# Optimization experiments

Measured on AMD Instinct MI355X. Metric: run time of the kernel, lower is better.

## Reference

```python
import jax, jax.numpy as jnp
import numpy as np

N, E, IN, C, H = 50000, 1600000, 128, 64, 2
HC = H * C  # 128; num_out = 128, conv_out channels per head = 64
NEG_SLOPE = 0.2


def setup_inputs() -> dict:
    key = jax.random.key(0)
    ks = jax.random.split(key, 16)
    x = jax.random.normal(ks[0], (N, IN), dtype=jnp.float32)
    edge_index = jax.random.randint(ks[1], (2, E), 0, N, dtype=jnp.int64)

    def gat_params(k, fan_in, heads, out_ch):
        k1, k2, k3 = jax.random.split(k, 3)
        sc = 1.0 / np.sqrt(fan_in)
        W = jax.random.normal(k1, (fan_in, heads * out_ch), dtype=jnp.float32) * sc
        a_src = jax.random.normal(k2, (heads, out_ch), dtype=jnp.float32) * 0.1
        a_dst = jax.random.normal(k3, (heads, out_ch), dtype=jnp.float32) * 0.1
        b = jnp.zeros((heads * out_ch,), dtype=jnp.float32)
        return W, a_src, a_dst, b

    W_in, a_src_in, a_dst_in, b_in = gat_params(ks[2], IN, H, C)
    # 2 hidden layers, stacked on leading axis
    Wh, ash, adh, bh = [], [], [], []
    for i in range(2):
        W, a_s, a_d, b = gat_params(ks[3 + i], HC, H, C)
        Wh.append(W); ash.append(a_s); adh.append(a_d); bh.append(b)
    W_h = jnp.stack(Wh); a_src_h = jnp.stack(ash)
    a_dst_h = jnp.stack(adh); b_h = jnp.stack(bh)
    W_out, a_src_out, a_dst_out, b_out = gat_params(ks[6], HC, H, C)
    return dict(x=x, edge_index=edge_index,
                W_in=W_in, a_src_in=a_src_in, a_dst_in=a_dst_in, b_in=b_in,
                W_h=W_h, a_src_h=a_src_h, a_dst_h=a_dst_h, b_h=b_h,
                W_out=W_out, a_src_out=a_src_out, a_dst_out=a_dst_out, b_out=b_out)


def gat_layer(xf, src, dst, W, a_src, a_dst, b, heads, out_ch):
    n = xf.shape[0]
    h = (xf @ W).reshape(n, heads, out_ch)              # [N,H,C]
    e_src = jnp.einsum('nhc,hc->nh', h, a_src)          # [N,H]
    e_dst = jnp.einsum('nhc,hc->nh', h, a_dst)
    e = jax.nn.leaky_relu(e_src[src] + e_dst[dst], NEG_SLOPE)  # [E',H]
    m = jax.ops.segment_max(e, dst, num_segments=n)     # softmax over edges per dst
    p = jnp.exp(e - m[dst])
    s = jax.ops.segment_sum(p, dst, num_segments=n)
    alpha = p / (s[dst] + 1e-16)
    out = jax.ops.segment_sum(alpha[:, :, None] * h[src], dst, num_segments=n)
    return out.reshape(n, heads * out_ch) + b


def reference(x, edge_index, W_in, a_src_in, a_dst_in, b_in,
              W_h, a_src_h, a_dst_h, b_h,
              W_out, a_src_out, a_dst_out, b_out):
    # add self loops (PyG GATConv default add_self_loops=True)
    loops = jnp.arange(N, dtype=edge_index.dtype)
    src = jnp.concatenate([edge_index[0], loops])
    dst = jnp.concatenate([edge_index[1], loops])

    h = jax.nn.relu(gat_layer(x, src, dst, W_in, a_src_in, a_dst_in, b_in, H, C))
    for i in range(2):
        h = jax.nn.relu(gat_layer(h, src, dst, W_h[i], a_src_h[i], a_dst_h[i], b_h[i], H, C))
    out = gat_layer(h, src, dst, W_out, a_src_out, a_dst_out, b_out, H, C)
    return out
```

## Files before the change

### kernel.cpp

```cpp
#include <hip/hip_runtime.h>

#define NNODES 50000
#define NEDGES 1600000
#define NEG_SLOPE 0.2f

#define SCAN_NB 256
#define SCAN_CH 196

#define MT_ROWS 64
#define NMT 782
#define GEMM_BLOCKS 768
#define COUNT_BLOCKS 256

typedef __attribute__((ext_vector_type(8))) short short8;
typedef __attribute__((ext_vector_type(4))) float f32x4;
typedef __attribute__((ext_vector_type(8))) _Float16 h16x8;
typedef __attribute__((ext_vector_type(8))) unsigned short us8;

static __device__ __forceinline__ unsigned short f2bf(float f) {
    unsigned u = __float_as_uint(f);
    unsigned r = u + 0x7FFFu + ((u >> 16) & 1u);
    return (unsigned short)(r >> 16);
}
static __device__ __forceinline__ float bf2f(unsigned short h) {
    return __uint_as_float(((unsigned)h) << 16);
}
static __device__ __forceinline__ unsigned short f2h(float f) {
    union { _Float16 x; unsigned short u; } c;
    c.x = (_Float16)f;
    return c.u;
}


__global__ __launch_bounds__(256) void k_bsum(const int* __restrict__ count,
                                              int* __restrict__ bsum) {
    __shared__ int red[4];
    int t = threadIdx.x, b = blockIdx.x;
    int idx = b * SCAN_CH + t;
    int v = (t < SCAN_CH && idx < NNODES) ? count[idx] + 1 : 0;
    #pragma unroll
    for (int m = 1; m <= 32; m <<= 1) v += __shfl_xor(v, m);
    if ((t & 63) == 0) red[t >> 6] = v;
    __syncthreads();
    if (t == 0) bsum[b] = red[0] + red[1] + red[2] + red[3];
}

__global__ __launch_bounds__(256) void k_bscan(const int* __restrict__ bsum,
                                               int* __restrict__ boff,
                                               int* __restrict__ row_ptr) {
    __shared__ int s[256];
    int t = threadIdx.x;
    int v = bsum[t];
    s[t] = v;
    __syncthreads();
    for (int off = 1; off < 256; off <<= 1) {
        int u = (t >= off) ? s[t - off] : 0;
        __syncthreads();
        s[t] += u;
        __syncthreads();
    }
    boff[t] = s[t] - v;
    if (t == 255) row_ptr[NNODES] = s[255];
}

__global__ __launch_bounds__(256) void k_rowptr(const int* __restrict__ count,
                                                const int* __restrict__ boff,
                                                int* __restrict__ row_ptr,
                                                int* __restrict__ csr_src) {
    __shared__ int s[256];
    int t = threadIdx.x, b = blockIdx.x;
    int idx = b * SCAN_CH + t;
    bool valid = (t < SCAN_CH && idx < NNODES);
    int v = valid ? count[idx] + 1 : 0;
    s[t] = v;
    __syncthreads();
    for (int off = 1; off < 256; off <<= 1) {
        int u = (t >= off) ? s[t - off] : 0;
        __syncthreads();
        s[t] += u;
        __syncthreads();
    }
    if (valid) {
        int run = boff[b] + s[t] - v;
        row_ptr[idx] = run;
        csr_src[run] = idx;
    }
}

__global__ void k_scatter(const int* __restrict__ ei, const int* __restrict__ row_ptr,
                          const int* __restrict__ pos, int* __restrict__ csr_src) {
    int t = blockIdx.x * blockDim.x + threadIdx.x;
    int stride = gridDim.x * blockDim.x;
    #pragma unroll
    for (int i = 0; i < 4; i++) {
        int e = t + i * stride;
        if (e < NEDGES) {
            int s = ei[e];
            int d = ei[NEDGES + e];
            __builtin_nontemporal_store(s, &csr_src[row_ptr[d] + 1 + pos[e]]);
        }
    }
}

__global__ __launch_bounds__(256) void k_wprep(const float* __restrict__ W0,
                                               const float* __restrict__ Wh,
                                               const float* __restrict__ Wout,
                                               unsigned short* __restrict__ wthi,
                                               unsigned short* __restrict__ wtlo) {
    int t = blockIdx.x * blockDim.x + threadIdx.x;
    int l = t >> 14;
    int i = t & 16383;
    int k = i >> 7, n = i & 127;
    const float* src = (l == 0) ? W0 : (l == 3) ? Wout : (Wh + (size_t)(l - 1) * 16384);
    float v = src[i];
    unsigned short h = f2bf(v);
    wthi[(size_t)l * 16384 + n * 128 + k] = h;
    wtlo[(size_t)l * 16384 + n * 128 + k] = f2bf(v - bf2f(h));
}

__global__ __launch_bounds__(256, 3) void k_gemm_mfma(
        const float* __restrict__ X,
        const unsigned short* __restrict__ Ahi, const unsigned short* __restrict__ Alo,
        const unsigned short* __restrict__ Wthi, const unsigned short* __restrict__ Wtlo,
        const float* __restrict__ a_src, const float* __restrict__ a_dst,
        unsigned short* __restrict__ Hh,
        float* __restrict__ e_src, float* __restrict__ e_dst, int use_x,
        const int* __restrict__ ei, int* __restrict__ count, int* __restrict__ pos)
{
    __shared__ __align__(16) short sAhi[MT_ROWS * 128];
    __shared__ __align__(16) short sAlo[MT_ROWS * 128];
    __shared__ float eS[4][MT_ROWS];
    __shared__ float eD[4][MT_ROWS];

    if (blockIdx.x >= GEMM_BLOCKS) {
        int t = (blockIdx.x - GEMM_BLOCKS) * 256 + threadIdx.x;
        for (int base = t; base < NEDGES; base += 8 * 65536) {
            #pragma unroll
            for (int i = 0; i < 8; i++) {
                int e = base + i * 65536;
                if (e < NEDGES) pos[e] = atomicAdd(&count[ei[NEDGES + e]], 1);
            }
        }
        return;
    }

    const int tid  = threadIdx.x;
    const int lane = tid & 63;
    const int w    = tid >> 6;
    const int l15  = lane & 15;
    const int quad = lane >> 4;

    short8 Bh[2][4], Bl[2][4];
    #pragma unroll
    for (int nt = 0; nt < 2; nt++) {
        int n = w * 32 + nt * 16 + l15;
        #pragma unroll
        for (int ks = 0; ks < 4; ks++) {
            Bh[nt][ks] = *(const short8*)(Wthi + (size_t)n * 128 + ks * 32 + quad * 8);
            Bl[nt][ks] = *(const short8*)(Wtlo + (size_t)n * 128 + ks * 32 + quad * 8);
        }
    }
    float as0 = a_src[w * 32 + l15],      ad0 = a_dst[w * 32 + l15];
    float as1 = a_src[w * 32 + 16 + l15], ad1 = a_dst[w * 32 + 16 + l15];

    for (int mt0 = blockIdx.x; mt0 < NMT; mt0 += GEMM_BLOCKS) {
        const int row0 = mt0 * MT_ROWS;

        for (int i = tid; i < MT_ROWS * 16; i += 256) {
            int m  = i >> 4;
            int kc = i & 15;
            int g  = row0 + m; if (g > NNODES - 1) g = NNODES - 1;
            int cp = kc ^ (m & 15);
            short8 vh, vl;
            if (use_x) {
                float4 xa = *(const float4*)(X + (size_t)g * 128 + kc * 8);
                float4 xb = *(const float4*)(X + (size_t)g * 128 + kc * 8 + 4);
                float xs[8] = {xa.x, xa.y, xa.z, xa.w, xb.x, xb.y, xb.z, xb.w};
                #pragma unroll
                for (int q = 0; q < 8; q++) {
                    unsigned short h = f2bf(xs[q]);
                    vh[q] = (short)h;
                    vl[q] = (short)f2bf(xs[q] - bf2f(h));
                }
            } else {
                vh = *(const short8*)(Ahi + (size_t)g * 128 + kc * 8);
                vl = *(const short8*)(Alo + (size_t)g * 128 + kc * 8);
            }
            *(short8*)&sAhi[m * 128 + cp * 8] = vh;
            *(short8*)&sAlo[m * 128 + cp * 8] = vl;
        }
        __syncthreads();

        f32x4 zero = {0.f, 0.f, 0.f, 0.f};
        f32x4 acc[4][2];
        #pragma unroll
        for (int mt = 0; mt < 4; mt++) { acc[mt][0] = zero; acc[mt][1] = zero; }
        #pragma unroll
        for (int mt = 0; mt < 4; mt++) {
            int m = mt * 16 + l15;
            #pragma unroll
            for (int ks = 0; ks < 4; ks++) {
                int kc = ks * 4 + quad;
                int cp = kc ^ l15;
                short8 ah = *(const short8*)&sAhi[m * 128 + cp * 8];
                short8 al = *(const short8*)&sAlo[m * 128 + cp * 8];
                #pragma unroll
                for (int nt = 0; nt < 2; nt++) {
                    acc[mt][nt] = __builtin_amdgcn_mfma_f32_16x16x32_bf16(ah, Bh[nt][ks], acc[mt][nt], 0, 0, 0);
                    acc[mt][nt] = __builtin_amdgcn_mfma_f32_16x16x32_bf16(al, Bh[nt][ks], acc[mt][nt], 0, 0, 0);
                    acc[mt][nt] = __builtin_amdgcn_mfma_f32_16x16x32_bf16(ah, Bl[nt][ks], acc[mt][nt], 0, 0, 0);
                }
            }
        }

        #pragma unroll
        for (int mt = 0; mt < 4; mt++) {
            #pragma unroll
            for (int r = 0; r < 4; r++) {
                int m = mt * 16 + quad * 4 + r;
                int g = row0 + m;
                float v0 = acc[mt][0][r], v1 = acc[mt][1][r];
                if (g < NNODES) {
                    int n0 = w * 32 + l15;
                    Hh[(size_t)g * 128 + n0]      = f2h(v0);
                    Hh[(size_t)g * 128 + n0 + 16] = f2h(v1);
                }
                float ps = v0 * as0 + v1 * as1;
                float pd = v0 * ad0 + v1 * ad1;
                ps += __shfl_xor(ps, 1); ps += __shfl_xor(ps, 2);
                ps += __shfl_xor(ps, 4); ps += __shfl_xor(ps, 8);
                pd += __shfl_xor(pd, 1); pd += __shfl_xor(pd, 2);
                pd += __shfl_xor(pd, 4); pd += __shfl_xor(pd, 8);
                if (l15 == 0) { eS[w][m] = ps; eD[w][m] = pd; }
            }
        }
        __syncthreads();
        if (tid < MT_ROWS * 2) {
            int m = tid >> 1, head = tid & 1;
            int g = row0 + m;
            if (g < NNODES) {
                e_src[g * 2 + head] = eS[head * 2][m] + eS[head * 2 + 1][m];
                e_dst[g * 2 + head] = eD[head * 2][m] + eD[head * 2 + 1][m];
            }
        }
        __syncthreads();
    }
}

template <int FINAL>
__device__ __forceinline__ void agg_body(const _Float16* __restrict__ Hh,
                                         const float* __restrict__ e_src,
                                         const float* __restrict__ e_dst,
                                         const int* __restrict__ row_ptr,
                                         const int* __restrict__ csr_src,
                                         const float* __restrict__ bias,
                                         float* __restrict__ outf,
                                         unsigned short* __restrict__ ohi,
                                         unsigned short* __restrict__ olo) {
    int lane = threadIdx.x & 63;
    int wv   = threadIdx.x >> 6;
    int d    = blockIdx.x * 4 + wv;
    if (d >= NNODES) return;
    int qt   = lane >> 4;
    int cl   = lane & 15;
    int head = cl >> 3;
    int c0   = cl * 8;
    float ed = e_dst[d * 2 + head];
    int beg = row_ptr[d], end = row_ptr[d + 1];
    float acc[8] = {0.f, 0.f, 0.f, 0.f, 0.f, 0.f, 0.f, 0.f};
    float ssum = 0.f;
    int j = beg;
    for (; j + 16 <= end; j += 16) {
        int s0 = csr_src[j + qt],      s1 = csr_src[j + 4 + qt];
        int s2 = csr_src[j + 8 + qt],  s3 = csr_src[j + 12 + qt];
        h16x8 h0 = *(const h16x8*)(Hh + (size_t)s0 * 128 + c0);
        h16x8 h1 = *(const h16x8*)(Hh + (size_t)s1 * 128 + c0);
        h16x8 h2 = *(const h16x8*)(Hh + (size_t)s2 * 128 + c0);
        h16x8 h3 = *(const h16x8*)(Hh + (size_t)s3 * 128 + c0);
        float t0 = e_src[s0 * 2 + head] + ed, t1 = e_src[s1 * 2 + head] + ed;
        float t2 = e_src[s2 * 2 + head] + ed, t3 = e_src[s3 * 2 + head] + ed;
        t0 = t0 > 0.f ? t0 : NEG_SLOPE * t0;  t1 = t1 > 0.f ? t1 : NEG_SLOPE * t1;
        t2 = t2 > 0.f ? t2 : NEG_SLOPE * t2;  t3 = t3 > 0.f ? t3 : NEG_SLOPE * t3;
        float p0 = __expf(t0), p1 = __expf(t1), p2 = __expf(t2), p3 = __expf(t3);
        #pragma unroll
        for (int c = 0; c < 8; c++)
            acc[c] += p0 * (float)h0[c] + p1 * (float)h1[c]
                    + p2 * (float)h2[c] + p3 * (float)h3[c];
        ssum += p0 + p1 + p2 + p3;
    }
    for (; j < end; j += 4) {
        int idx = j + qt;
        bool valid = idx < end;
        int s = csr_src[valid ? idx : end - 1];
        float t = e_src[s * 2 + head] + ed;
        t = t > 0.f ? t : NEG_SLOPE * t;
        float p = valid ? __expf(t) : 0.f;
        h16x8 hq = *(const h16x8*)(Hh + (size_t)s * 128 + c0);
        #pragma unroll
        for (int c = 0; c < 8; c++) acc[c] += p * (float)hq[c];
        ssum += p;
    }
    #pragma unroll
    for (int c = 0; c < 8; c++) {
        acc[c] += __shfl_xor(acc[c], 16);
        acc[c] += __shfl_xor(acc[c], 32);
    }
    ssum += __shfl_xor(ssum, 16);
    ssum += __shfl_xor(ssum, 32);
    if (qt == 0) {
        float inv = 1.0f / ssum;
        f32x4 b0 = *(const f32x4*)(bias + c0);
        f32x4 b1 = *(const f32x4*)(bias + c0 + 4);
        float o[8];
        #pragma unroll
        for (int c = 0; c < 8; c++) {
            float bv = (c < 4) ? b0[c] : b1[c - 4];
            o[c] = acc[c] * inv + bv;
        }
        if (FINAL) {
            f32x4 w0 = {o[0], o[1], o[2], o[3]};
            f32x4 w1 = {o[4], o[5], o[6], o[7]};
            *(f32x4*)(outf + (size_t)d * 128 + c0)     = w0;
            *(f32x4*)(outf + (size_t)d * 128 + c0 + 4) = w1;
        } else {
            us8 vh, vl;
            #pragma unroll
            for (int c = 0; c < 8; c++) {
                float oc = fmaxf(o[c], 0.f);
                unsigned short hbits = f2bf(oc);
                vh[c] = hbits;
                vl[c] = f2bf(oc - bf2f(hbits));
            }
            *(us8*)&ohi[(size_t)d * 128 + c0] = vh;
            *(us8*)&olo[(size_t)d * 128 + c0] = vl;
        }
    }
}

__global__ __launch_bounds__(256) void k_aggregate_h(const unsigned short* __restrict__ Hh,
                                                     const float* __restrict__ e_src,
                                                     const float* __restrict__ e_dst,
                                                     const int* __restrict__ row_ptr,
                                                     const int* __restrict__ csr_src,
                                                     const float* __restrict__ bias,
                                                     unsigned short* __restrict__ ohi,
                                                     unsigned short* __restrict__ olo) {
    agg_body<0>((const _Float16*)Hh, e_src, e_dst, row_ptr, csr_src, bias,
                nullptr, ohi, olo);
}

__global__ __launch_bounds__(256) void k_aggregate_f(const unsigned short* __restrict__ Hh,
                                                     const float* __restrict__ e_src,
                                                     const float* __restrict__ e_dst,
                                                     const int* __restrict__ row_ptr,
                                                     const int* __restrict__ csr_src,
                                                     const float* __restrict__ bias,
                                                     float* __restrict__ outf) {
    agg_body<1>((const _Float16*)Hh, e_src, e_dst, row_ptr, csr_src, bias,
                outf, nullptr, nullptr);
}


extern "C" void kernel_launch(void* const* d_in, const int* in_sizes, int n_in,
                              void* d_out, int out_size, void* d_ws, size_t ws_size,
                              hipStream_t stream) {
    const float* x  = (const float*)d_in[0];
    const int*   ei = (const int*)d_in[1];

    char* ws = (char*)d_ws;
    size_t off = 0;
    auto alloc = [&](size_t bytes) {
        void* p = ws + off;
        off = (off + bytes + 255) & ~(size_t)255;
        return p;
    };
    int*            count   = (int*)alloc((size_t)NNODES * 4);
    int*            row_ptr = (int*)alloc((size_t)(NNODES + 1) * 4);
    int*            csr     = (int*)alloc((size_t)(NEDGES + NNODES) * 4);
    int*            pos     = (int*)alloc((size_t)NEDGES * 4);
    int*            bsum    = (int*)alloc((size_t)SCAN_NB * 4);
    int*            boff    = (int*)alloc((size_t)SCAN_NB * 4);
    unsigned short* hh      = (unsigned short*)alloc((size_t)NNODES * 128 * 2);
    unsigned short* wthi    = (unsigned short*)alloc((size_t)4 * 16384 * 2);
    unsigned short* wtlo    = (unsigned short*)alloc((size_t)4 * 16384 * 2);
    float*          es      = (float*)alloc((size_t)NNODES * 2 * 4);
    float*          edv     = (float*)alloc((size_t)NNODES * 2 * 4);
    (void)ws_size; (void)in_sizes; (void)n_in; (void)out_size;

    unsigned short* hi = (unsigned short*)d_out;
    unsigned short* lo = hi + (size_t)NNODES * 128;

    const float* W0   = (const float*)d_in[2];
    const float* W_h  = (const float*)d_in[6];
    const float* Wout = (const float*)d_in[10];

    const float* ash = (const float*)d_in[7];
    const float* adh = (const float*)d_in[8];
    const float* bh  = (const float*)d_in[9];

    struct Layer { const float *as, *ad, *b; };
    Layer L[4] = {
        { (const float*)d_in[3],  (const float*)d_in[4],  (const float*)d_in[5]  },
        { ash,        adh,        bh        },
        { ash + 128,  adh + 128,  bh + 128  },
        { (const float*)d_in[11], (const float*)d_in[12], (const float*)d_in[13] },
    };

    hipMemsetAsync(count, 0, (size_t)NNODES * 4, stream);
    k_wprep<<<256, 256, 0, stream>>>(W0, W_h, Wout, wthi, wtlo);

    const int agg_blocks = (NNODES + 3) / 4;
    for (int l = 0; l < 4; l++) {
        int grid = (l == 0) ? GEMM_BLOCKS + COUNT_BLOCKS : GEMM_BLOCKS;
        k_gemm_mfma<<<grid, 256, 0, stream>>>(
            x, hi, lo, wthi + (size_t)l * 16384, wtlo + (size_t)l * 16384,
            L[l].as, L[l].ad, hh, es, edv, l == 0 ? 1 : 0, ei, count, pos);
        if (l == 0) {
            k_bsum   <<<SCAN_NB, 256, 0, stream>>>(count, bsum);
            k_bscan  <<<1, 256, 0, stream>>>(bsum, boff, row_ptr);
            k_rowptr <<<SCAN_NB, 256, 0, stream>>>(count, boff, row_ptr, csr);
            k_scatter<<<(NEDGES + 4 * 256 - 1) / (4 * 256), 256, 0, stream>>>(ei, row_ptr, pos, csr);
        }
        if (l < 3) {
            k_aggregate_h<<<agg_blocks, 256, 0, stream>>>(hh, es, edv, row_ptr, csr,
                                                          L[l].b, hi, lo);
        } else {
            k_aggregate_f<<<agg_blocks, 256, 0, stream>>>(hh, es, edv, row_ptr, csr,
                                                          L[l].b, (float*)d_out);
        }
    }
}
```

Measured before the change: 537.6 us.

## Pad degree counters per cache line and partition CSR scatter by destination range

Each per-node atomic counter now sits in its own 64-byte slot, so atomics on neighbouring nodes no longer contend on one cache line. The CSR scatter now splits edges into slices with eight blocks each, and each block writes only edges whose destination falls in one eighth of the node range. This keeps each block's scattered writes within a narrower region of the CSR array to improve cache locality. The cost is a 16x larger counter buffer and memset, strided counter reads in the scan kernels, and every block reading the dst array eight times over.

```diff
diff --git a/kernel.cpp b/kernel.cpp
--- a/kernel.cpp
+++ b/kernel.cpp
@@ -11,6 +11,12 @@
 #define NMT 782
 #define GEMM_BLOCKS 768
 #define COUNT_BLOCKS 256
+
+#define SCAT_GROUPS 512
+#define SLICE ((NEDGES + SCAT_GROUPS - 1) / SCAT_GROUPS)
+#define DPART (NNODES / 8)
+
+#define CPAD 4
 
 typedef __attribute__((ext_vector_type(8))) short short8;
 typedef __attribute__((ext_vector_type(4))) float f32x4;
@@ -37,7 +43,7 @@
     __shared__ int red[4];
     int t = threadIdx.x, b = blockIdx.x;
     int idx = b * SCAN_CH + t;
-    int v = (t < SCAN_CH && idx < NNODES) ? count[idx] + 1 : 0;
+    int v = (t < SCAN_CH && idx < NNODES) ? count[idx << CPAD] + 1 : 0;
     #pragma unroll
     for (int m = 1; m <= 32; m <<= 1) v += __shfl_xor(v, m);
     if ((t & 63) == 0) red[t >> 6] = v;
@@ -71,7 +77,7 @@
     int t = threadIdx.x, b = blockIdx.x;
     int idx = b * SCAN_CH + t;
     bool valid = (t < SCAN_CH && idx < NNODES);
-    int v = valid ? count[idx] + 1 : 0;
+    int v = valid ? count[idx << CPAD] + 1 : 0;
     s[t] = v;
     __syncthreads();
     for (int off = 1; off < 256; off <<= 1) {
@@ -87,17 +93,21 @@
     }
 }
 
-__global__ void k_scatter(const int* __restrict__ ei, const int* __restrict__ row_ptr,
-                          const int* __restrict__ pos, int* __restrict__ csr_src) {
-    int t = blockIdx.x * blockDim.x + threadIdx.x;
-    int stride = gridDim.x * blockDim.x;
-    #pragma unroll
-    for (int i = 0; i < 4; i++) {
-        int e = t + i * stride;
-        if (e < NEDGES) {
+__global__ __launch_bounds__(256) void k_scatter(const int* __restrict__ ei,
+                                                 const int* __restrict__ row_ptr,
+                                                 const int* __restrict__ pos,
+                                                 int* __restrict__ csr_src) {
+    int grp  = blockIdx.x >> 3;
+    int part = blockIdx.x & 7;
+    int lo = grp * SLICE;
+    int hi = lo + SLICE; if (hi > NEDGES) hi = NEDGES;
+    int dlo = part * DPART;
+    int dhi = dlo + DPART;
+    for (int e = lo + threadIdx.x; e < hi; e += 256) {
+        int d = ei[NEDGES + e];
+        if (d >= dlo && d < dhi) {
             int s = ei[e];
-            int d = ei[NEDGES + e];
-            __builtin_nontemporal_store(s, &csr_src[row_ptr[d] + 1 + pos[e]]);
+            csr_src[row_ptr[d] + 1 + pos[e]] = s;
         }
     }
 }
@@ -138,7 +148,7 @@
             #pragma unroll
             for (int i = 0; i < 8; i++) {
                 int e = base + i * 65536;
-                if (e < NEDGES) pos[e] = atomicAdd(&count[ei[NEDGES + e]], 1);
+                if (e < NEDGES) pos[e] = atomicAdd(&count[ei[NEDGES + e] << CPAD], 1);
             }
         }
         return;
@@ -374,7 +384,7 @@
         off = (off + bytes + 255) & ~(size_t)255;
         return p;
     };
-    int*            count   = (int*)alloc((size_t)NNODES * 4);
+    int*            count   = (int*)alloc((size_t)NNODES * 64);
     int*            row_ptr = (int*)alloc((size_t)(NNODES + 1) * 4);
     int*            csr     = (int*)alloc((size_t)(NEDGES + NNODES) * 4);
     int*            pos     = (int*)alloc((size_t)NEDGES * 4);
@@ -406,7 +416,7 @@
         { (const float*)d_in[11], (const float*)d_in[12], (const float*)d_in[13] },
     };
 
-    hipMemsetAsync(count, 0, (size_t)NNODES * 4, stream);
+    hipMemsetAsync(count, 0, (size_t)NNODES * 64, stream);
     k_wprep<<<256, 256, 0, stream>>>(W0, W_h, Wout, wthi, wtlo);
 
     const int agg_blocks = (NNODES + 3) / 4;
@@ -419,7 +429,7 @@
             k_bsum   <<<SCAN_NB, 256, 0, stream>>>(count, bsum);
             k_bscan  <<<1, 256, 0, stream>>>(bsum, boff, row_ptr);
             k_rowptr <<<SCAN_NB, 256, 0, stream>>>(count, boff, row_ptr, csr);
-            k_scatter<<<(NEDGES + 4 * 256 - 1) / (4 * 256), 256, 0, stream>>>(ei, row_ptr, pos, csr);
+            k_scatter<<<SCAT_GROUPS * 8, 256, 0, stream>>>(ei, row_ptr, pos, csr);
         }
         if (l < 3) {
             k_aggregate_h<<<agg_blocks, 256, 0, stream>>>(hh, es, edv, row_ptr, csr,
```

After: 511.9 us. -4.8%, faster.
